# Kernel optimization log

Hardware: AMD Instinct MI355X
Metric: run time of the kernel (lower is better)

The kernel has to match this reference:

```python
import jax, jax.numpy as jnp
import numpy as np

INNER_STEPS = 50
INNER_LR = 0.1
Y_MEAN = 0.0


def _mlp(params, inp):
    # eqx.nn.MLP(in=3, out=1, width=64, depth=3): relu hidden, identity final
    W1, b1, W2, b2, W3, b3, W4, b4 = params
    h = jax.nn.relu(W1 @ inp + b1)
    h = jax.nn.relu(W2 @ h + b2)
    h = jax.nn.relu(W3 @ h + b3)
    return jnp.squeeze(W4 @ h + b4)


def setup_inputs() -> dict:
    key = jax.random.key(0)
    ks = jax.random.split(key, 10)
    B, CD, W = 8192, 1, 64
    d_in = 2 + CD
    x = jax.random.normal(ks[0], (B, 1), dtype=jnp.float32)
    c = jax.random.normal(ks[1], (B, CD), dtype=jnp.float32)
    def lin(k, fan_out, fan_in):
        lim = 1.0 / np.sqrt(fan_in)
        kw, kb = jax.random.split(k)
        Wm = jax.random.uniform(kw, (fan_out, fan_in), minval=-lim, maxval=lim, dtype=jnp.float32)
        bm = jax.random.uniform(kb, (fan_out,), minval=-lim, maxval=lim, dtype=jnp.float32)
        return Wm, bm
    W1, b1 = lin(ks[2], W, d_in)
    W2, b2 = lin(ks[3], W, W)
    W3, b3 = lin(ks[4], W, W)
    W4, b4 = lin(ks[5], 1, W)
    return {"x": x, "c": c, "W1": W1, "b1": b1, "W2": W2, "b2": b2,
            "W3": W3, "b3": b3, "W4": W4, "b4": b4}


def reference(x, c, W1, b1, W2, b2, W3, b3, W4, b4):
    params = (W1, b1, W2, b2, W3, b3, W4, b4)
    # nearest-neighbor c0 per sample (excluding self)
    dists = jnp.linalg.norm(c[:, None, :] - c[None, :, :], axis=-1)  # [B,B]
    dists = dists + jnp.eye(dists.shape[0], dtype=dists.dtype) * 1e9
    c0 = c[jnp.argmin(dists, axis=1)]  # [B,CD]

    def base_energy(xi, yi, ci):
        return _mlp(params, jnp.concatenate([xi, yi, ci], axis=0))

    def solve(xi, ci, c0i):
        y0 = jnp.array([Y_MEAN], dtype=xi.dtype)

        def step(y, _):
            def loss(yy):
                E0, dE = jax.jvp(lambda cc: base_energy(xi, yy, cc), (c0i,), (ci - c0i,))
                return E0 + dE
            gy = jax.grad(loss)(y)
            return y - INNER_LR * gy, None

        yf, _ = jax.lax.scan(step, y0, None, length=INNER_STEPS)
        return yf

    return jax.vmap(solve)(x, c, c0)  # [B,1]
```

## Files before the change

### kernel.cpp

```cpp
#include <hip/hip_runtime.h>

#define BATCH 8192
#define LOSC  2048.0f
#define LOINV (1.0f / 2048.0f)

typedef _Float16 f16x4 __attribute__((ext_vector_type(4)));
typedef __fp16   fp16x2 __attribute__((ext_vector_type(2)));
typedef float    f32x4 __attribute__((ext_vector_type(4)));

union PK2 { fp16x2 h; unsigned u; };
union U4  { f16x4 v; unsigned u[2]; };

__device__ __forceinline__ unsigned pkrtz(float a, float b) {
    PK2 p; p.h = __builtin_amdgcn_cvt_pkrtz(a, b); return p.u;
}
__device__ __forceinline__ float lo0(unsigned hp, float v) {
    PK2 p; p.u = hp; return (v - (float)p.h[0]) * LOSC;
}
__device__ __forceinline__ float lo1(unsigned hp, float v) {
    PK2 p; p.u = hp; return (v - (float)p.h[1]) * LOSC;
}

__global__ __launch_bounds__(256) void nn_kernel(const float* __restrict__ c,
                                                 float* __restrict__ c0) {
    __shared__ float cs[BATCH];
    const int t = threadIdx.x;
    {
        const float4* cg = (const float4*)c;
        float4* cl = (float4*)cs;
        for (int j = t; j < BATCH / 4; j += 256) cl[j] = cg[j];
    }
    __syncthreads();
    const int part = t & 31;
    const int i    = blockIdx.x * 8 + (t >> 5);
    const float ci = cs[i];
    const int sj0 = ((i & 3) == 0) ? (i >> 2) : -1;
    const int sj1 = ((i & 3) == 1) ? (i >> 2) : -1;
    const int sj2 = ((i & 3) == 2) ? (i >> 2) : -1;
    const int sj3 = ((i & 3) == 3) ? (i >> 2) : -1;
    const float4* cs4 = (const float4*)cs;
    float bd0 = 3e38f, bd1 = 3e38f, bd2 = 3e38f, bd3 = 3e38f;
    int   bj0 = 0,     bj1 = 0,     bj2 = 0,     bj3 = 0;
    #pragma unroll 4
    for (int tt = 0; tt < 64; ++tt) {
        const int jj = part + (tt << 5);
        const float4 v = cs4[jj];
        float d0 = fabsf(ci - v.x);
        float d1 = fabsf(ci - v.y);
        float d2 = fabsf(ci - v.z);
        float d3 = fabsf(ci - v.w);
        if (jj == sj0) d0 = 3e38f;
        if (jj == sj1) d1 = 3e38f;
        if (jj == sj2) d2 = 3e38f;
        if (jj == sj3) d3 = 3e38f;
        if (d0 < bd0) { bd0 = d0; bj0 = jj; }
        if (d1 < bd1) { bd1 = d1; bj1 = jj; }
        if (d2 < bd2) { bd2 = d2; bj2 = jj; }
        if (d3 < bd3) { bd3 = d3; bj3 = jj; }
    }
    float best = bd0; int bestj = bj0 * 4 + 0;
    { const int j1 = bj1 * 4 + 1; if (bd1 < best || (bd1 == best && j1 < bestj)) { best = bd1; bestj = j1; } }
    { const int j2 = bj2 * 4 + 2; if (bd2 < best || (bd2 == best && j2 < bestj)) { best = bd2; bestj = j2; } }
    { const int j3 = bj3 * 4 + 3; if (bd3 < best || (bd3 == best && j3 < bestj)) { best = bd3; bestj = j3; } }
    #pragma unroll
    for (int off = 1; off < 32; off <<= 1) {
        const float od = __shfl_xor(best, off);
        const int   oj = __shfl_xor(bestj, off);
        if (od < best || (od == best && oj < bestj)) { best = od; bestj = oj; }
    }
    if (part == 0) c0[i] = cs[bestj];
}

__global__ __launch_bounds__(64, 1) void solve_kernel(
    const float* __restrict__ x, const float* __restrict__ c0g,
    const float* __restrict__ W1, const float* __restrict__ b1,
    const float* __restrict__ W2, const float* __restrict__ b2,
    const float* __restrict__ W3, const float* __restrict__ b3,
    const float* __restrict__ W4, float* __restrict__ out)
{
    const int lane = threadIdx.x & 63;
    const int q  = lane >> 4;
    const int cc = lane & 15;
    const bool fwd = (cc < 8);
    const int s = cc & 7;
    const int sbase = blockIdx.x * 8;

    f16x4 W2h[4][4], W2l[4][4], W3h[4][4], W3l[4][4];
    #pragma unroll
    for (int T = 0; T < 4; ++T)
        #pragma unroll
        for (int m = 0; m < 4; ++m) {
            const int off = (T * 16 + cc) * 64 + m * 16 + q * 4;
            const float4 w2 = *(const float4*)(W2 + off);
            const float4 w3 = *(const float4*)(W3 + off);
            U4 h, l;
            h.u[0] = pkrtz(w2.x, w2.y); h.u[1] = pkrtz(w2.z, w2.w);
            l.u[0] = pkrtz(lo0(h.u[0], w2.x), lo1(h.u[0], w2.y));
            l.u[1] = pkrtz(lo0(h.u[1], w2.z), lo1(h.u[1], w2.w));
            W2h[T][m] = h.v; W2l[T][m] = l.v;
            h.u[0] = pkrtz(w3.x, w3.y); h.u[1] = pkrtz(w3.z, w3.w);
            l.u[0] = pkrtz(lo0(h.u[0], w3.x), lo1(h.u[0], w3.y));
            l.u[1] = pkrtz(lo0(h.u[1], w3.z), lo1(h.u[1], w3.w));
            W3h[T][m] = h.v; W3l[T][m] = l.v;
        }

    float b2m[16], b3m[16], w4r[16];
    #pragma unroll
    for (int T = 0; T < 4; ++T)
        #pragma unroll
        for (int r = 0; r < 4; ++r) {
            const int row = T * 16 + q * 4 + r;
            b2m[T * 4 + r] = fwd ? b2[row] : 0.f;
            b3m[T * 4 + r] = fwd ? b3[row] : 0.f;
            w4r[T * 4 + r] = W4[row];
        }

    float A1v[16], w11v[16];
    {
        const float xs  = x[sbase + s];
        const float c0s = c0g[sbase + s];
        #pragma unroll
        for (int m = 0; m < 4; ++m)
            #pragma unroll
            for (int j = 0; j < 4; ++j) {
                const int k = m * 16 + q * 4 + j;
                w11v[m * 4 + j] = W1[k * 3 + 1];
                A1v[m * 4 + j]  = fmaf(xs, W1[k * 3 + 0],
                                       fmaf(c0s, W1[k * 3 + 2], b1[k]));
            }
    }

    float y = 0.0f;

    #pragma unroll 1
    for (int step = 0; step < 50; ++step) {
        U4 B1h[4], B1l[4];
        #pragma unroll
        for (int m = 0; m < 4; ++m) {
            float v[4];
            #pragma unroll
            for (int j = 0; j < 4; ++j) {
                const float w = w11v[m * 4 + j];
                const float z = fmaf(y, w, A1v[m * 4 + j]);
                v[j] = fwd ? fmaxf(z, 0.f) : (z > 0.f ? w : 0.f);
            }
            const unsigned h0 = pkrtz(v[0], v[1]);
            const unsigned h1 = pkrtz(v[2], v[3]);
            B1h[m].u[0] = h0; B1h[m].u[1] = h1;
            B1l[m].u[0] = pkrtz(lo0(h0, v[0]), lo1(h0, v[1]));
            B1l[m].u[1] = pkrtz(lo0(h1, v[2]), lo1(h1, v[3]));
        }
        f32x4 ZH[4], ZL[4];
        #pragma unroll
        for (int T = 0; T < 4; ++T) {
            f32x4 aH;
            aH[0] = b2m[T * 4 + 0]; aH[1] = b2m[T * 4 + 1];
            aH[2] = b2m[T * 4 + 2]; aH[3] = b2m[T * 4 + 3];
            f32x4 aLa = {0.f, 0.f, 0.f, 0.f};
            f32x4 aLb = {0.f, 0.f, 0.f, 0.f};
            #pragma unroll
            for (int m = 0; m < 4; ++m) {
                aH  = __builtin_amdgcn_mfma_f32_16x16x16f16(W2h[T][m], B1h[m].v, aH, 0, 0, 0);
                aLa = __builtin_amdgcn_mfma_f32_16x16x16f16(W2h[T][m], B1l[m].v, aLa, 0, 0, 0);
                aLb = __builtin_amdgcn_mfma_f32_16x16x16f16(W2l[T][m], B1h[m].v, aLb, 0, 0, 0);
            }
            ZH[T] = aH; ZL[T] = aLa + aLb;
        }
        U4 B2h[4], B2l[4];
        #pragma unroll
        for (int T = 0; T < 4; ++T) {
            float v[4];
            #pragma unroll
            for (int r = 0; r < 4; ++r) {
                const float z = fmaf(ZL[T][r], LOINV, ZH[T][r]);
                const float recv = __shfl_xor(z, 8);
                v[r] = fwd ? fmaxf(z, 0.f) : (recv > 0.f ? z : 0.f);
            }
            const unsigned h0 = pkrtz(v[0], v[1]);
            const unsigned h1 = pkrtz(v[2], v[3]);
            B2h[T].u[0] = h0; B2h[T].u[1] = h1;
            B2l[T].u[0] = pkrtz(lo0(h0, v[0]), lo1(h0, v[1]));
            B2l[T].u[1] = pkrtz(lo0(h1, v[2]), lo1(h1, v[3]));
        }
        #pragma unroll
        for (int T = 0; T < 4; ++T) {
            f32x4 aH;
            aH[0] = b3m[T * 4 + 0]; aH[1] = b3m[T * 4 + 1];
            aH[2] = b3m[T * 4 + 2]; aH[3] = b3m[T * 4 + 3];
            f32x4 aLa = {0.f, 0.f, 0.f, 0.f};
            f32x4 aLb = {0.f, 0.f, 0.f, 0.f};
            #pragma unroll
            for (int m = 0; m < 4; ++m) {
                aH  = __builtin_amdgcn_mfma_f32_16x16x16f16(W3h[T][m], B2h[m].v, aH, 0, 0, 0);
                aLa = __builtin_amdgcn_mfma_f32_16x16x16f16(W3h[T][m], B2l[m].v, aLa, 0, 0, 0);
                aLb = __builtin_amdgcn_mfma_f32_16x16x16f16(W3l[T][m], B2h[m].v, aLb, 0, 0, 0);
            }
            ZH[T] = aH; ZL[T] = aLa + aLb;
        }
        float g = 0.f;
        #pragma unroll
        for (int T = 0; T < 4; ++T)
            #pragma unroll
            for (int r = 0; r < 4; ++r) {
                const float z = fmaf(ZL[T][r], LOINV, ZH[T][r]);
                const float recv  = __shfl_xor(z, 8);
                const float maskv = fwd ? z : recv;
                const float valv  = fwd ? recv : z;
                g = fmaf(w4r[T * 4 + r], (maskv > 0.f) ? valv : 0.f, g);
            }
        const float r1 = __shfl_xor(g, 16);
        const float r2 = __shfl_xor(g, 32);
        const float r3 = __shfl_xor(g, 48);
        y -= 0.1f * ((g + r1) + (r2 + r3));
    }
    if (lane < 8) out[sbase + lane] = y;
}

extern "C" void kernel_launch(void* const* d_in, const int* in_sizes, int n_in,
                              void* d_out, int out_size, void* d_ws, size_t ws_size,
                              hipStream_t stream) {
    const float* x  = (const float*)d_in[0];
    const float* c  = (const float*)d_in[1];
    const float* W1 = (const float*)d_in[2];
    const float* b1 = (const float*)d_in[3];
    const float* W2 = (const float*)d_in[4];
    const float* b2 = (const float*)d_in[5];
    const float* W3 = (const float*)d_in[6];
    const float* b3 = (const float*)d_in[7];
    const float* W4 = (const float*)d_in[8];
    float* c0  = (float*)d_ws;
    float* out = (float*)d_out;

    nn_kernel<<<BATCH / 8, 256, 0, stream>>>(c, c0);
    solve_kernel<<<BATCH / 8, 64, 0, stream>>>(x, c0, W1, b1, W2, b2, W3, b3, W4, out);
}
```

Before: 175.0 us.

## Split solve kernel K-dimension across two waves with LDS partial-sum exchange

Each 8-sample block now runs on two wavefronts instead of one. Each wave holds half of the W2/W3 K-slices and computes partial 64-row MFMA products. The partial sums for the other wave's output tiles go through shared memory, and the gradient reduction is combined through LDS after a barrier. The aim is to halve the serial MFMA chain per inner step and use more SIMDs. The cost is three __syncthreads per step plus LDS round-trips, which add latency to a dependency-bound loop.

```diff
diff --git a/kernel.cpp b/kernel.cpp
--- a/kernel.cpp
+++ b/kernel.cpp
@@ -71,26 +71,32 @@
     if (part == 0) c0[i] = cs[bestj];
 }
 
-__global__ __launch_bounds__(64, 1) void solve_kernel(
+__global__ __launch_bounds__(128, 2) void solve_kernel(
     const float* __restrict__ x, const float* __restrict__ c0g,
     const float* __restrict__ W1, const float* __restrict__ b1,
     const float* __restrict__ W2, const float* __restrict__ b2,
     const float* __restrict__ W3, const float* __restrict__ b3,
     const float* __restrict__ W4, float* __restrict__ out)
 {
-    const int lane = threadIdx.x & 63;
+    __shared__ __align__(16) float pbuf2[4][64][4];
+    __shared__ __align__(16) float pbuf3[4][64][4];
+    __shared__ float gbuf[2][16];
+
+    const int tid  = threadIdx.x;
+    const int w    = tid >> 6;
+    const int lane = tid & 63;
     const int q  = lane >> 4;
     const int cc = lane & 15;
     const bool fwd = (cc < 8);
     const int s = cc & 7;
     const int sbase = blockIdx.x * 8;
 
-    f16x4 W2h[4][4], W2l[4][4], W3h[4][4], W3l[4][4];
+    f16x4 W2h[4][2], W2l[4][2], W3h[4][2], W3l[4][2];
     #pragma unroll
     for (int T = 0; T < 4; ++T)
         #pragma unroll
-        for (int m = 0; m < 4; ++m) {
-            const int off = (T * 16 + cc) * 64 + m * 16 + q * 4;
+        for (int m = 0; m < 2; ++m) {
+            const int off = (T * 16 + cc) * 64 + (w * 2 + m) * 16 + q * 4;
             const float4 w2 = *(const float4*)(W2 + off);
             const float4 w3 = *(const float4*)(W3 + off);
             U4 h, l;
@@ -104,26 +110,26 @@
             W3h[T][m] = h.v; W3l[T][m] = l.v;
         }
 
-    float b2m[16], b3m[16], w4r[16];
+    float b2m[8], b3m[8], w4r[8];
     #pragma unroll
-    for (int T = 0; T < 4; ++T)
+    for (int i = 0; i < 2; ++i)
         #pragma unroll
         for (int r = 0; r < 4; ++r) {
-            const int row = T * 16 + q * 4 + r;
-            b2m[T * 4 + r] = fwd ? b2[row] : 0.f;
-            b3m[T * 4 + r] = fwd ? b3[row] : 0.f;
-            w4r[T * 4 + r] = W4[row];
-        }
-
-    float A1v[16], w11v[16];
+            const int row = (2 * w + i) * 16 + q * 4 + r;
+            b2m[i * 4 + r] = fwd ? b2[row] : 0.f;
+            b3m[i * 4 + r] = fwd ? b3[row] : 0.f;
+            w4r[i * 4 + r] = W4[row];
+        }
+
+    float A1v[8], w11v[8];
     {
         const float xs  = x[sbase + s];
         const float c0s = c0g[sbase + s];
         #pragma unroll
-        for (int m = 0; m < 4; ++m)
+        for (int m = 0; m < 2; ++m)
             #pragma unroll
             for (int j = 0; j < 4; ++j) {
-                const int k = m * 16 + q * 4 + j;
+                const int k = (w * 2 + m) * 16 + q * 4 + j;
                 w11v[m * 4 + j] = W1[k * 3 + 1];
                 A1v[m * 4 + j]  = fmaf(xs, W1[k * 3 + 0],
                                        fmaf(c0s, W1[k * 3 + 2], b1[k]));
@@ -134,15 +140,15 @@
 
     #pragma unroll 1
     for (int step = 0; step < 50; ++step) {
-        U4 B1h[4], B1l[4];
-        #pragma unroll
-        for (int m = 0; m < 4; ++m) {
+        U4 B1h[2], B1l[2];
+        #pragma unroll
+        for (int m = 0; m < 2; ++m) {
             float v[4];
             #pragma unroll
             for (int j = 0; j < 4; ++j) {
-                const float w = w11v[m * 4 + j];
-                const float z = fmaf(y, w, A1v[m * 4 + j]);
-                v[j] = fwd ? fmaxf(z, 0.f) : (z > 0.f ? w : 0.f);
+                const float ww = w11v[m * 4 + j];
+                const float z = fmaf(y, ww, A1v[m * 4 + j]);
+                v[j] = fwd ? fmaxf(z, 0.f) : (z > 0.f ? ww : 0.f);
             }
             const unsigned h0 = pkrtz(v[0], v[1]);
             const unsigned h1 = pkrtz(v[2], v[3]);
@@ -153,67 +159,107 @@
         f32x4 ZH[4], ZL[4];
         #pragma unroll
         for (int T = 0; T < 4; ++T) {
-            f32x4 aH;
-            aH[0] = b2m[T * 4 + 0]; aH[1] = b2m[T * 4 + 1];
-            aH[2] = b2m[T * 4 + 2]; aH[3] = b2m[T * 4 + 3];
+            f32x4 aH  = {0.f, 0.f, 0.f, 0.f};
             f32x4 aLa = {0.f, 0.f, 0.f, 0.f};
             f32x4 aLb = {0.f, 0.f, 0.f, 0.f};
             #pragma unroll
-            for (int m = 0; m < 4; ++m) {
+            for (int m = 0; m < 2; ++m) {
                 aH  = __builtin_amdgcn_mfma_f32_16x16x16f16(W2h[T][m], B1h[m].v, aH, 0, 0, 0);
                 aLa = __builtin_amdgcn_mfma_f32_16x16x16f16(W2h[T][m], B1l[m].v, aLa, 0, 0, 0);
                 aLb = __builtin_amdgcn_mfma_f32_16x16x16f16(W2l[T][m], B1h[m].v, aLb, 0, 0, 0);
             }
             ZH[T] = aH; ZL[T] = aLa + aLb;
         }
-        U4 B2h[4], B2l[4];
-        #pragma unroll
-        for (int T = 0; T < 4; ++T) {
+        #pragma unroll
+        for (int i = 0; i < 2; ++i) {
+            const int To = 2 * (1 - w) + i;
+            float4 pv;
+            pv.x = fmaf(ZL[To][0], LOINV, ZH[To][0]);
+            pv.y = fmaf(ZL[To][1], LOINV, ZH[To][1]);
+            pv.z = fmaf(ZL[To][2], LOINV, ZH[To][2]);
+            pv.w = fmaf(ZL[To][3], LOINV, ZH[To][3]);
+            *(float4*)&pbuf2[To][lane][0] = pv;
+        }
+        __syncthreads();
+        float z2[8], rc2[8];
+        #pragma unroll
+        for (int i = 0; i < 2; ++i) {
+            const int T = 2 * w + i;
+            const float4 po = *(const float4*)&pbuf2[T][lane][0];
+            z2[i * 4 + 0] = (fmaf(ZL[T][0], LOINV, ZH[T][0]) + po.x) + b2m[i * 4 + 0];
+            z2[i * 4 + 1] = (fmaf(ZL[T][1], LOINV, ZH[T][1]) + po.y) + b2m[i * 4 + 1];
+            z2[i * 4 + 2] = (fmaf(ZL[T][2], LOINV, ZH[T][2]) + po.z) + b2m[i * 4 + 2];
+            z2[i * 4 + 3] = (fmaf(ZL[T][3], LOINV, ZH[T][3]) + po.w) + b2m[i * 4 + 3];
+        }
+        #pragma unroll
+        for (int k = 0; k < 8; ++k) rc2[k] = __shfl_xor(z2[k], 8);
+        U4 B2h[2], B2l[2];
+        #pragma unroll
+        for (int i = 0; i < 2; ++i) {
             float v[4];
             #pragma unroll
             for (int r = 0; r < 4; ++r) {
-                const float z = fmaf(ZL[T][r], LOINV, ZH[T][r]);
-                const float recv = __shfl_xor(z, 8);
-                v[r] = fwd ? fmaxf(z, 0.f) : (recv > 0.f ? z : 0.f);
+                const float z = z2[i * 4 + r];
+                v[r] = fwd ? fmaxf(z, 0.f) : (rc2[i * 4 + r] > 0.f ? z : 0.f);
             }
             const unsigned h0 = pkrtz(v[0], v[1]);
             const unsigned h1 = pkrtz(v[2], v[3]);
-            B2h[T].u[0] = h0; B2h[T].u[1] = h1;
-            B2l[T].u[0] = pkrtz(lo0(h0, v[0]), lo1(h0, v[1]));
-            B2l[T].u[1] = pkrtz(lo0(h1, v[2]), lo1(h1, v[3]));
+            B2h[i].u[0] = h0; B2h[i].u[1] = h1;
+            B2l[i].u[0] = pkrtz(lo0(h0, v[0]), lo1(h0, v[1]));
+            B2l[i].u[1] = pkrtz(lo0(h1, v[2]), lo1(h1, v[3]));
         }
         #pragma unroll
         for (int T = 0; T < 4; ++T) {
-            f32x4 aH;
-            aH[0] = b3m[T * 4 + 0]; aH[1] = b3m[T * 4 + 1];
-            aH[2] = b3m[T * 4 + 2]; aH[3] = b3m[T * 4 + 3];
+            f32x4 aH  = {0.f, 0.f, 0.f, 0.f};
             f32x4 aLa = {0.f, 0.f, 0.f, 0.f};
             f32x4 aLb = {0.f, 0.f, 0.f, 0.f};
             #pragma unroll
-            for (int m = 0; m < 4; ++m) {
+            for (int m = 0; m < 2; ++m) {
                 aH  = __builtin_amdgcn_mfma_f32_16x16x16f16(W3h[T][m], B2h[m].v, aH, 0, 0, 0);
                 aLa = __builtin_amdgcn_mfma_f32_16x16x16f16(W3h[T][m], B2l[m].v, aLa, 0, 0, 0);
                 aLb = __builtin_amdgcn_mfma_f32_16x16x16f16(W3l[T][m], B2h[m].v, aLb, 0, 0, 0);
             }
             ZH[T] = aH; ZL[T] = aLa + aLb;
         }
+        #pragma unroll
+        for (int i = 0; i < 2; ++i) {
+            const int To = 2 * (1 - w) + i;
+            float4 pv;
+            pv.x = fmaf(ZL[To][0], LOINV, ZH[To][0]);
+            pv.y = fmaf(ZL[To][1], LOINV, ZH[To][1]);
+            pv.z = fmaf(ZL[To][2], LOINV, ZH[To][2]);
+            pv.w = fmaf(ZL[To][3], LOINV, ZH[To][3]);
+            *(float4*)&pbuf3[To][lane][0] = pv;
+        }
+        __syncthreads();
+        float z3[8], rc3[8];
+        #pragma unroll
+        for (int i = 0; i < 2; ++i) {
+            const int T = 2 * w + i;
+            const float4 po = *(const float4*)&pbuf3[T][lane][0];
+            z3[i * 4 + 0] = (fmaf(ZL[T][0], LOINV, ZH[T][0]) + po.x) + b3m[i * 4 + 0];
+            z3[i * 4 + 1] = (fmaf(ZL[T][1], LOINV, ZH[T][1]) + po.y) + b3m[i * 4 + 1];
+            z3[i * 4 + 2] = (fmaf(ZL[T][2], LOINV, ZH[T][2]) + po.z) + b3m[i * 4 + 2];
+            z3[i * 4 + 3] = (fmaf(ZL[T][3], LOINV, ZH[T][3]) + po.w) + b3m[i * 4 + 3];
+        }
+        #pragma unroll
+        for (int k = 0; k < 8; ++k) rc3[k] = __shfl_xor(z3[k], 8);
         float g = 0.f;
         #pragma unroll
-        for (int T = 0; T < 4; ++T)
-            #pragma unroll
-            for (int r = 0; r < 4; ++r) {
-                const float z = fmaf(ZL[T][r], LOINV, ZH[T][r]);
-                const float recv  = __shfl_xor(z, 8);
-                const float maskv = fwd ? z : recv;
-                const float valv  = fwd ? recv : z;
-                g = fmaf(w4r[T * 4 + r], (maskv > 0.f) ? valv : 0.f, g);
-            }
+        for (int k = 0; k < 8; ++k) {
+            const float maskv = fwd ? z3[k] : rc3[k];
+            const float valv  = fwd ? rc3[k] : z3[k];
+            g = fmaf(w4r[k], (maskv > 0.f) ? valv : 0.f, g);
+        }
         const float r1 = __shfl_xor(g, 16);
         const float r2 = __shfl_xor(g, 32);
         const float r3 = __shfl_xor(g, 48);
-        y -= 0.1f * ((g + r1) + (r2 + r3));
-    }
-    if (lane < 8) out[sbase + lane] = y;
+        const float gq = (g + r1) + (r2 + r3);
+        if (lane < 16) gbuf[w][lane] = gq;
+        __syncthreads();
+        y -= 0.1f * (gbuf[0][cc] + gbuf[1][cc]);
+    }
+    if (w == 0 && lane < 8) out[sbase + lane] = y;
 }
 
 extern "C" void kernel_launch(void* const* d_in, const int* in_sizes, int n_in,
@@ -232,5 +278,5 @@
     float* out = (float*)d_out;
 
     nn_kernel<<<BATCH / 8, 256, 0, stream>>>(c, c0);
-    solve_kernel<<<BATCH / 8, 64, 0, stream>>>(x, c0, W1, b1, W2, b2, W3, b3, W4, out);
-}
+    solve_kernel<<<BATCH / 8, 128, 0, stream>>>(x, c0, W1, b1, W2, b2, W3, b3, W4, out);
+}
```

After: 419.1 us. 2.39x slower.

## Switch to 16x16x32 f16 MFMA with cross-lane operand reshuffle between layers

Applied to the files above, without the earlier changes.

Replaces the 16x16x16 f16 MFMAs with the K=32 variant, which halves the MFMA instruction count per layer. It regroups the weight and layer-1 activation fragments into 8-element chunks. The layer-2 output no longer lines up with the K=32 B-operand layout, so packed halves are now redistributed with ds_bpermute shuffles. The xor shuffles are also batched before use to expose more parallelism, at the cost of extra permute traffic and register pressure.

```diff
diff --git a/kernel.cpp b/kernel.cpp
--- a/kernel.cpp
+++ b/kernel.cpp
@@ -4,12 +4,12 @@
 #define LOSC  2048.0f
 #define LOINV (1.0f / 2048.0f)
 
-typedef _Float16 f16x4 __attribute__((ext_vector_type(4)));
+typedef _Float16 f16x8 __attribute__((ext_vector_type(8)));
 typedef __fp16   fp16x2 __attribute__((ext_vector_type(2)));
 typedef float    f32x4 __attribute__((ext_vector_type(4)));
 
 union PK2 { fp16x2 h; unsigned u; };
-union U4  { f16x4 v; unsigned u[2]; };
+union U8  { f16x8 v; unsigned u[4]; };
 
 __device__ __forceinline__ unsigned pkrtz(float a, float b) {
     PK2 p; p.h = __builtin_amdgcn_cvt_pkrtz(a, b); return p.u;
@@ -85,23 +85,30 @@
     const int s = cc & 7;
     const int sbase = blockIdx.x * 8;
 
-    f16x4 W2h[4][4], W2l[4][4], W3h[4][4], W3l[4][4];
+    f16x8 W2h[4][2], W2l[4][2], W3h[4][2], W3l[4][2];
     #pragma unroll
     for (int T = 0; T < 4; ++T)
         #pragma unroll
-        for (int m = 0; m < 4; ++m) {
-            const int off = (T * 16 + cc) * 64 + m * 16 + q * 4;
-            const float4 w2 = *(const float4*)(W2 + off);
-            const float4 w3 = *(const float4*)(W3 + off);
-            U4 h, l;
-            h.u[0] = pkrtz(w2.x, w2.y); h.u[1] = pkrtz(w2.z, w2.w);
-            l.u[0] = pkrtz(lo0(h.u[0], w2.x), lo1(h.u[0], w2.y));
-            l.u[1] = pkrtz(lo0(h.u[1], w2.z), lo1(h.u[1], w2.w));
-            W2h[T][m] = h.v; W2l[T][m] = l.v;
-            h.u[0] = pkrtz(w3.x, w3.y); h.u[1] = pkrtz(w3.z, w3.w);
-            l.u[0] = pkrtz(lo0(h.u[0], w3.x), lo1(h.u[0], w3.y));
-            l.u[1] = pkrtz(lo0(h.u[1], w3.z), lo1(h.u[1], w3.w));
-            W3h[T][m] = h.v; W3l[T][m] = l.v;
+        for (int ch = 0; ch < 2; ++ch) {
+            const float* p2 = W2 + (T * 16 + cc) * 64 + ch * 32 + q * 8;
+            const float* p3 = W3 + (T * 16 + cc) * 64 + ch * 32 + q * 8;
+            const float4 a2 = *(const float4*)p2, b2v = *(const float4*)(p2 + 4);
+            const float4 a3 = *(const float4*)p3, b3v = *(const float4*)(p3 + 4);
+            U8 h, l;
+            h.u[0] = pkrtz(a2.x, a2.y);   h.u[1] = pkrtz(a2.z, a2.w);
+            h.u[2] = pkrtz(b2v.x, b2v.y); h.u[3] = pkrtz(b2v.z, b2v.w);
+            l.u[0] = pkrtz(lo0(h.u[0], a2.x), lo1(h.u[0], a2.y));
+            l.u[1] = pkrtz(lo0(h.u[1], a2.z), lo1(h.u[1], a2.w));
+            l.u[2] = pkrtz(lo0(h.u[2], b2v.x), lo1(h.u[2], b2v.y));
+            l.u[3] = pkrtz(lo0(h.u[3], b2v.z), lo1(h.u[3], b2v.w));
+            W2h[T][ch] = h.v; W2l[T][ch] = l.v;
+            h.u[0] = pkrtz(a3.x, a3.y);   h.u[1] = pkrtz(a3.z, a3.w);
+            h.u[2] = pkrtz(b3v.x, b3v.y); h.u[3] = pkrtz(b3v.z, b3v.w);
+            l.u[0] = pkrtz(lo0(h.u[0], a3.x), lo1(h.u[0], a3.y));
+            l.u[1] = pkrtz(lo0(h.u[1], a3.z), lo1(h.u[1], a3.w));
+            l.u[2] = pkrtz(lo0(h.u[2], b3v.x), lo1(h.u[2], b3v.y));
+            l.u[3] = pkrtz(lo0(h.u[3], b3v.z), lo1(h.u[3], b3v.w));
+            W3h[T][ch] = h.v; W3l[T][ch] = l.v;
         }
 
     float b2m[16], b3m[16], w4r[16];
@@ -120,35 +127,40 @@
         const float xs  = x[sbase + s];
         const float c0s = c0g[sbase + s];
         #pragma unroll
-        for (int m = 0; m < 4; ++m)
-            #pragma unroll
-            for (int j = 0; j < 4; ++j) {
-                const int k = m * 16 + q * 4 + j;
-                w11v[m * 4 + j] = W1[k * 3 + 1];
-                A1v[m * 4 + j]  = fmaf(xs, W1[k * 3 + 0],
-                                       fmaf(c0s, W1[k * 3 + 2], b1[k]));
-            }
-    }
+        for (int ch = 0; ch < 2; ++ch)
+            #pragma unroll
+            for (int j = 0; j < 8; ++j) {
+                const int k = ch * 32 + q * 8 + j;
+                w11v[ch * 8 + j] = W1[k * 3 + 1];
+                A1v[ch * 8 + j]  = fmaf(xs, W1[k * 3 + 0],
+                                        fmaf(c0s, W1[k * 3 + 2], b1[k]));
+            }
+    }
+
+    const int srcA = ((q & 1) * 2) * 16 + cc;
+    const int srcB = srcA + 16;
+    const bool hiT = (q >> 1) != 0;
 
     float y = 0.0f;
 
     #pragma unroll 1
     for (int step = 0; step < 50; ++step) {
-        U4 B1h[4], B1l[4];
-        #pragma unroll
-        for (int m = 0; m < 4; ++m) {
-            float v[4];
-            #pragma unroll
-            for (int j = 0; j < 4; ++j) {
-                const float w = w11v[m * 4 + j];
-                const float z = fmaf(y, w, A1v[m * 4 + j]);
+        U8 B1h[2], B1l[2];
+        #pragma unroll
+        for (int ch = 0; ch < 2; ++ch) {
+            float v[8];
+            #pragma unroll
+            for (int j = 0; j < 8; ++j) {
+                const float w = w11v[ch * 8 + j];
+                const float z = fmaf(y, w, A1v[ch * 8 + j]);
                 v[j] = fwd ? fmaxf(z, 0.f) : (z > 0.f ? w : 0.f);
             }
-            const unsigned h0 = pkrtz(v[0], v[1]);
-            const unsigned h1 = pkrtz(v[2], v[3]);
-            B1h[m].u[0] = h0; B1h[m].u[1] = h1;
-            B1l[m].u[0] = pkrtz(lo0(h0, v[0]), lo1(h0, v[1]));
-            B1l[m].u[1] = pkrtz(lo0(h1, v[2]), lo1(h1, v[3]));
+            #pragma unroll
+            for (int p = 0; p < 4; ++p) {
+                const unsigned hp = pkrtz(v[2 * p], v[2 * p + 1]);
+                B1h[ch].u[p] = hp;
+                B1l[ch].u[p] = pkrtz(lo0(hp, v[2 * p]), lo1(hp, v[2 * p + 1]));
+            }
         }
         f32x4 ZH[4], ZL[4];
         #pragma unroll
@@ -159,29 +171,53 @@
             f32x4 aLa = {0.f, 0.f, 0.f, 0.f};
             f32x4 aLb = {0.f, 0.f, 0.f, 0.f};
             #pragma unroll
-            for (int m = 0; m < 4; ++m) {
-                aH  = __builtin_amdgcn_mfma_f32_16x16x16f16(W2h[T][m], B1h[m].v, aH, 0, 0, 0);
-                aLa = __builtin_amdgcn_mfma_f32_16x16x16f16(W2h[T][m], B1l[m].v, aLa, 0, 0, 0);
-                aLb = __builtin_amdgcn_mfma_f32_16x16x16f16(W2l[T][m], B1h[m].v, aLb, 0, 0, 0);
+            for (int ch = 0; ch < 2; ++ch) {
+                aH  = __builtin_amdgcn_mfma_f32_16x16x32_f16(W2h[T][ch], B1h[ch].v, aH, 0, 0, 0);
+                aLa = __builtin_amdgcn_mfma_f32_16x16x32_f16(W2h[T][ch], B1l[ch].v, aLa, 0, 0, 0);
+                aLb = __builtin_amdgcn_mfma_f32_16x16x32_f16(W2l[T][ch], B1h[ch].v, aLb, 0, 0, 0);
             }
             ZH[T] = aH; ZL[T] = aLa + aLb;
         }
-        U4 B2h[4], B2l[4];
+        float z2[16], rc2[16];
+        #pragma unroll
+        for (int k = 0; k < 16; ++k)
+            z2[k] = fmaf(ZL[k >> 2][k & 3], LOINV, ZH[k >> 2][k & 3]);
+        #pragma unroll
+        for (int k = 0; k < 16; ++k)
+            rc2[k] = __shfl_xor(z2[k], 8);
+        unsigned pkh[4][2], pkl[4][2];
         #pragma unroll
         for (int T = 0; T < 4; ++T) {
             float v[4];
             #pragma unroll
             for (int r = 0; r < 4; ++r) {
-                const float z = fmaf(ZL[T][r], LOINV, ZH[T][r]);
-                const float recv = __shfl_xor(z, 8);
-                v[r] = fwd ? fmaxf(z, 0.f) : (recv > 0.f ? z : 0.f);
+                const float z = z2[T * 4 + r];
+                v[r] = fwd ? fmaxf(z, 0.f) : (rc2[T * 4 + r] > 0.f ? z : 0.f);
             }
             const unsigned h0 = pkrtz(v[0], v[1]);
             const unsigned h1 = pkrtz(v[2], v[3]);
-            B2h[T].u[0] = h0; B2h[T].u[1] = h1;
-            B2l[T].u[0] = pkrtz(lo0(h0, v[0]), lo1(h0, v[1]));
-            B2l[T].u[1] = pkrtz(lo0(h1, v[2]), lo1(h1, v[3]));
-        }
+            pkh[T][0] = h0; pkh[T][1] = h1;
+            pkl[T][0] = pkrtz(lo0(h0, v[0]), lo1(h0, v[1]));
+            pkl[T][1] = pkrtz(lo0(h1, v[2]), lo1(h1, v[3]));
+        }
+        U8 B2h[2], B2l[2];
+        #pragma unroll
+        for (int ch = 0; ch < 2; ++ch)
+            #pragma unroll
+            for (int p = 0; p < 2; ++p) {
+                const unsigned haL = (unsigned)__shfl((int)pkh[ch * 2][p],     srcA);
+                const unsigned haH = (unsigned)__shfl((int)pkh[ch * 2 + 1][p], srcA);
+                const unsigned hbL = (unsigned)__shfl((int)pkh[ch * 2][p],     srcB);
+                const unsigned hbH = (unsigned)__shfl((int)pkh[ch * 2 + 1][p], srcB);
+                const unsigned laL = (unsigned)__shfl((int)pkl[ch * 2][p],     srcA);
+                const unsigned laH = (unsigned)__shfl((int)pkl[ch * 2 + 1][p], srcA);
+                const unsigned lbL = (unsigned)__shfl((int)pkl[ch * 2][p],     srcB);
+                const unsigned lbH = (unsigned)__shfl((int)pkl[ch * 2 + 1][p], srcB);
+                B2h[ch].u[p]     = hiT ? haH : haL;
+                B2h[ch].u[2 + p] = hiT ? hbH : hbL;
+                B2l[ch].u[p]     = hiT ? laH : laL;
+                B2l[ch].u[2 + p] = hiT ? lbH : lbL;
+            }
         #pragma unroll
         for (int T = 0; T < 4; ++T) {
             f32x4 aH;
@@ -190,24 +226,27 @@
             f32x4 aLa = {0.f, 0.f, 0.f, 0.f};
             f32x4 aLb = {0.f, 0.f, 0.f, 0.f};
             #pragma unroll
-            for (int m = 0; m < 4; ++m) {
-                aH  = __builtin_amdgcn_mfma_f32_16x16x16f16(W3h[T][m], B2h[m].v, aH, 0, 0, 0);
-                aLa = __builtin_amdgcn_mfma_f32_16x16x16f16(W3h[T][m], B2l[m].v, aLa, 0, 0, 0);
-                aLb = __builtin_amdgcn_mfma_f32_16x16x16f16(W3l[T][m], B2h[m].v, aLb, 0, 0, 0);
+            for (int ch = 0; ch < 2; ++ch) {
+                aH  = __builtin_amdgcn_mfma_f32_16x16x32_f16(W3h[T][ch], B2h[ch].v, aH, 0, 0, 0);
+                aLa = __builtin_amdgcn_mfma_f32_16x16x32_f16(W3h[T][ch], B2l[ch].v, aLa, 0, 0, 0);
+                aLb = __builtin_amdgcn_mfma_f32_16x16x32_f16(W3l[T][ch], B2h[ch].v, aLb, 0, 0, 0);
             }
             ZH[T] = aH; ZL[T] = aLa + aLb;
         }
+        float z3[16], rc3[16];
+        #pragma unroll
+        for (int k = 0; k < 16; ++k)
+            z3[k] = fmaf(ZL[k >> 2][k & 3], LOINV, ZH[k >> 2][k & 3]);
+        #pragma unroll
+        for (int k = 0; k < 16; ++k)
+            rc3[k] = __shfl_xor(z3[k], 8);
         float g = 0.f;
         #pragma unroll
-        for (int T = 0; T < 4; ++T)
-            #pragma unroll
-            for (int r = 0; r < 4; ++r) {
-                const float z = fmaf(ZL[T][r], LOINV, ZH[T][r]);
-                const float recv  = __shfl_xor(z, 8);
-                const float maskv = fwd ? z : recv;
-                const float valv  = fwd ? recv : z;
-                g = fmaf(w4r[T * 4 + r], (maskv > 0.f) ? valv : 0.f, g);
-            }
+        for (int k = 0; k < 16; ++k) {
+            const float maskv = fwd ? z3[k] : rc3[k];
+            const float valv  = fwd ? rc3[k] : z3[k];
+            g = fmaf(w4r[k], (maskv > 0.f) ? valv : 0.f, g);
+        }
         const float r1 = __shfl_xor(g, 16);
         const float r2 = __shfl_xor(g, 32);
         const float r3 = __shfl_xor(g, 48);
```

After: 178.4 us. No clear change (+1.9%).
